# Kernel optimization log

Hardware: AMD Instinct MI355X
Metric: run time of the kernel (lower is better)

Reference implementation:

```python
import jax, jax.numpy as jnp
import numpy as np

H = 1024          # hidden_size
C = 4             # residual_channels
RH = 16           # residual_heads
HS = H // RH      # head_size for residual (64)
DR = 8            # delta_rank
M = 4096          # mlp_size
NH = 16           # attention heads
HD = H // NH      # attention head dim (64)
A_SIZE = (C - 1) * RH   # 48
B_SIZE = C * RH         # 64
EPS = 1e-5
SSM_EPS = 1e-5


def rat_read(res, W, gamma, beta, num_outputs):
    # res: [b,l,H*C]; W: [H, num_outputs, C] (Conv1d groups=H)
    b, l, _ = res.shape
    x = res.reshape(b, l, H, C)
    y = jnp.einsum('blhc,hoc->bloh', x, W)            # [b,l,o,H]
    mu = y.mean(-1, keepdims=True)
    var = y.var(-1, keepdims=True)
    yn = (y - mu) * jax.lax.rsqrt(var + EPS)          # GroupNorm: each group = one output
    yn = yn * gamma.reshape(num_outputs, H) + beta.reshape(num_outputs, H)
    return yn.reshape(b, l, num_outputs * H)


def rope(x, pos):
    # x: [b,l,NH,HD], pos: [b,l]
    half = HD // 2
    inv = 1.0 / (10000.0 ** (jnp.arange(half, dtype=jnp.float32) / half))
    ang = pos.astype(jnp.float32)[..., None] * inv    # [b,l,half]
    cos = jnp.cos(ang)[:, :, None, :]
    sin = jnp.sin(ang)[:, :, None, :]
    x1, x2 = x[..., :half], x[..., half:]
    return jnp.concatenate([x1 * cos - x2 * sin, x2 * cos + x1 * sin], axis=-1)


def attention(qkv_in, qkv_w, pos):
    # qkv_in: [b,l,3H]; qkv_w: [3,H,H] (grouped 1x1 conv = 3 independent linears)
    b, l, _ = qkv_in.shape
    q, k, v = jnp.split(qkv_in, 3, axis=-1)
    q = jnp.einsum('bli,oi->blo', q, qkv_w[0]).reshape(b, l, NH, HD)
    k = jnp.einsum('bli,oi->blo', k, qkv_w[1]).reshape(b, l, NH, HD)
    v = jnp.einsum('bli,oi->blo', v, qkv_w[2]).reshape(b, l, NH, HD)
    q = rope(q, pos)
    k = rope(k, pos)
    scores = jnp.einsum('bqhd,bkhd->bhqk', q, k) / np.sqrt(HD).astype(np.float32)
    mask = jnp.tril(jnp.ones((l, l), dtype=bool))
    scores = jnp.where(mask, scores, jnp.float32(-1e30))
    p = jax.nn.softmax(scores, axis=-1)
    o = jnp.einsum('bhqk,bkhd->bqhd', p, v)
    return o.reshape(b, l, H)  # get_o is identity (no output proj)


def rat_write(res, y, wod_w, wab_w, wab_b, du_w, du_b):
    # res: [b,l,H*C], y: [b,l,y_size]
    b, l, _ = res.shape
    o_d = y @ wod_w.T                                 # [b,l,H+DR]
    A_B = y @ wab_w.T + wab_b                         # [b,l,A+B]
    out = o_d[..., :H]
    delta_low = o_d[..., H:]
    A_logit = A_B[..., :A_SIZE]
    B_proj = A_B[..., A_SIZE:2 * A_SIZE]
    B_skip = A_B[..., 2 * A_SIZE:]
    delta = jax.nn.softplus(delta_low @ du_w.T + du_b)  # [b,l,H]
    hs = res.reshape(b, l, HS, RH, C)
    out = out.reshape(b, l, HS, RH, 1)
    delta = delta.reshape(b, l, HS, RH, 1)
    A_logit = A_logit.reshape(b, l, 1, RH, C - 1)
    B_proj = B_proj.reshape(b, l, 1, RH, C - 1)
    B_skip = B_skip.reshape(b, l, 1, RH, 1)
    A_neg = -jax.nn.softplus(A_logit)
    A_bar = jnp.exp(delta * A_neg)
    B_bar = (A_bar - 1.0) / (A_neg - SSM_EPS) * B_proj
    B_bar_skip = delta * B_skip
    A_full = jnp.concatenate([A_bar, jnp.ones_like(A_bar[..., :1])], axis=-1)
    B_full = jnp.concatenate([B_bar, B_bar_skip], axis=-1)
    return (hs * A_full + out * B_full).reshape(b, l, H * C)


def layer_forward(hidden_states, position_ids, attn_read_w, attn_read_g, attn_read_b,
                  qkv_w, attn_wod_w, attn_wab_w, attn_wab_b, attn_du_w, attn_du_b,
                  mlp_read_w, mlp_read_g, mlp_read_b, mlp_in_w,
                  mlp_wod_w, mlp_wab_w, mlp_wab_b, mlp_du_w, mlp_du_b):
    qkv_in = rat_read(hidden_states, attn_read_w, attn_read_g, attn_read_b, 3)
    attn_out = attention(qkv_in, qkv_w, position_ids)
    hidden_states = rat_write(hidden_states, attn_out, attn_wod_w, attn_wab_w,
                              attn_wab_b, attn_du_w, attn_du_b)
    mlp_in = rat_read(hidden_states, mlp_read_w, mlp_read_g, mlp_read_b, 2)
    g_in, u_in = mlp_in[..., :H], mlp_in[..., H:]
    gate = jnp.einsum('bli,oi->blo', g_in, mlp_in_w[0])
    up = jnp.einsum('bli,oi->blo', u_in, mlp_in_w[1])
    mlp_out = jax.nn.silu(gate) * up                  # [b,l,M]
    hidden_states = rat_write(hidden_states, mlp_out, mlp_wod_w, mlp_wab_w,
                              mlp_wab_b, mlp_du_w, mlp_du_b)
    return hidden_states


def setup_inputs() -> dict:
    key = jax.random.key(0)
    ks = jax.random.split(key, 20)
    B, L = 2, 2048
    s = 0.02
    return {
        'hidden_states': jax.random.normal(ks[0], (B, L, H * C), jnp.float32),
        'position_ids': jnp.tile(jnp.arange(L, dtype=jnp.int64), (B, 1)),
        'attn_read_w': jax.random.normal(ks[1], (H, 3, C), jnp.float32) / np.sqrt(C).astype(np.float32),
        'attn_read_g': jnp.ones((3 * H,), jnp.float32),
        'attn_read_b': jnp.zeros((3 * H,), jnp.float32),
        'qkv_w': jax.random.normal(ks[2], (3, H, H), jnp.float32) * s,
        'attn_wod_w': jax.random.normal(ks[3], (H + DR, H), jnp.float32) * s,
        'attn_wab_w': jax.random.normal(ks[4], (A_SIZE + B_SIZE, H), jnp.float32) * s,
        'attn_wab_b': jax.random.normal(ks[5], (A_SIZE + B_SIZE,), jnp.float32) * s,
        'attn_du_w': jax.random.normal(ks[6], (H, DR), jnp.float32) * s,
        'attn_du_b': jax.random.normal(ks[7], (H,), jnp.float32) * s,
        'mlp_read_w': jax.random.normal(ks[8], (H, 2, C), jnp.float32) / np.sqrt(C).astype(np.float32),
        'mlp_read_g': jnp.ones((2 * H,), jnp.float32),
        'mlp_read_b': jnp.zeros((2 * H,), jnp.float32),
        'mlp_in_w': jax.random.normal(ks[9], (2, M, H), jnp.float32) * s,
        'mlp_wod_w': jax.random.normal(ks[10], (H + DR, M), jnp.float32) * s,
        'mlp_wab_w': jax.random.normal(ks[11], (A_SIZE + B_SIZE, M), jnp.float32) * s,
        'mlp_wab_b': jax.random.normal(ks[12], (A_SIZE + B_SIZE,), jnp.float32) * s,
        'mlp_du_w': jax.random.normal(ks[13], (H, DR), jnp.float32) * s,
        'mlp_du_b': jax.random.normal(ks[14], (H,), jnp.float32) * s,
    }


def reference(hidden_states, position_ids, attn_read_w, attn_read_g, attn_read_b,
              qkv_w, attn_wod_w, attn_wab_w, attn_wab_b, attn_du_w, attn_du_b,
              mlp_read_w, mlp_read_g, mlp_read_b, mlp_in_w,
              mlp_wod_w, mlp_wab_w, mlp_wab_b, mlp_du_w, mlp_du_b):
    return layer_forward(hidden_states, position_ids, attn_read_w, attn_read_g,
                         attn_read_b, qkv_w, attn_wod_w, attn_wab_w, attn_wab_b,
                         attn_du_w, attn_du_b, mlp_read_w, mlp_read_g, mlp_read_b,
                         mlp_in_w, mlp_wod_w, mlp_wab_w, mlp_wab_b, mlp_du_w, mlp_du_b)
```

## Files before the change

### kernel.cpp

```cpp
#include <hip/hip_runtime.h>
#include <hip/hip_bf16.h>
#include <math.h>
#include <stdint.h>


constexpr int NTOK = 4096;

typedef __attribute__((ext_vector_type(8))) short short8_t;
typedef __attribute__((ext_vector_type(4))) float f32x4;

__device__ __forceinline__ ushort f2bf(float f) {
    union { float f; uint32_t u; } v; v.f = f;
    uint32_t r = v.u + 0x7fffu + ((v.u >> 16) & 1u);
    return (ushort)(r >> 16);
}
__device__ __forceinline__ float bf2f(ushort b) {
    union { uint32_t u; float f; } v; v.u = ((uint32_t)b) << 16;
    return v.f;
}
__device__ __forceinline__ uint32_t pack2(float lo, float hi) {
    union { __hip_bfloat162 h; uint32_t u; } v;
    v.h = __float22bfloat162_rn(make_float2(lo, hi));
    return v.u;
}
__device__ __forceinline__ float softplus_f(float x) {
    return (x > 20.0f) ? x : log1pf(expf(x));
}

__device__ __forceinline__ void gload_lds16(const void* g, void* l) {
    __builtin_amdgcn_global_load_lds(
        (const __attribute__((address_space(1))) uint32_t*)g,
        (__attribute__((address_space(3))) uint32_t*)l,
        16, 0, 0);
}

__global__ __launch_bounds__(256) void convert_flat_kernel(
    const float* __restrict__ src, ushort* __restrict__ dst)
{
    const size_t i = ((size_t)blockIdx.x * 256 + threadIdx.x) * 8;
    const float4 a = *(const float4*)(src + i);
    const float4 b = *(const float4*)(src + i + 4);
    union { ushort u[8]; uint4 v; } o;
    o.u[0] = f2bf(a.x); o.u[1] = f2bf(a.y); o.u[2] = f2bf(a.z); o.u[3] = f2bf(a.w);
    o.u[4] = f2bf(b.x); o.u[5] = f2bf(b.y); o.u[6] = f2bf(b.z); o.u[7] = f2bf(b.w);
    *(uint4*)(dst + i) = o.v;
}

__global__ __launch_bounds__(256) void rope_tab_kernel(float2* __restrict__ tab)
{
    const int idx = blockIdx.x * 256 + threadIdx.x;
    const int i = idx & 31;
    const int pos = idx >> 5;
    const float inv = expf(-(float)i * (9.210340371976184f / 32.0f));
    float s, c;
    sincosf((float)pos * inv, &s, &c);
    tab[idx] = make_float2(c, s);
}

__global__ __launch_bounds__(256) void build_comb_kernel(
    const float* __restrict__ wod, const float* __restrict__ wab,
    ushort* __restrict__ dst, int K)
{
    const size_t i = ((size_t)blockIdx.x * 256 + threadIdx.x) * 8;
    const int row = (int)(i / (size_t)K);
    const int col = (int)(i % (size_t)K);
    const float* src = nullptr;
    if (row < 1024)      src = wod + (size_t)row * K + col;
    else if (row < 1136) src = wab + (size_t)(row - 1024) * K + col;
    else if (row < 1144) src = wod + (size_t)(1024 + row - 1136) * K + col;
    union { ushort u[8]; uint4 v; } o;
    if (src) {
        const float4 a = *(const float4*)(src);
        const float4 b = *(const float4*)(src + 4);
        o.u[0] = f2bf(a.x); o.u[1] = f2bf(a.y); o.u[2] = f2bf(a.z); o.u[3] = f2bf(a.w);
        o.u[4] = f2bf(b.x); o.u[5] = f2bf(b.y); o.u[6] = f2bf(b.z); o.u[7] = f2bf(b.w);
    } else {
        o.v = make_uint4(0, 0, 0, 0);
    }
    *(uint4*)(dst + i) = o.v;
}

template <int NO>
__global__ __launch_bounds__(256) void rat_read_kernel(
    const float* __restrict__ res, const float* __restrict__ W,
    const float* __restrict__ gamma, const float* __restrict__ beta,
    ushort* __restrict__ out)
{
    const int t = blockIdx.x;
    const int tid = threadIdx.x;
    const float* rp = res + (size_t)t * 4096;
    float y[4][NO];
#pragma unroll
    for (int i = 0; i < 4; ++i) {
        const int h = tid + 256 * i;
        const float4 x = *(const float4*)(rp + h * 4);
#pragma unroll
        for (int o = 0; o < NO; ++o) {
            const float4 w = *(const float4*)(W + ((size_t)h * NO + o) * 4);
            y[i][o] = x.x * w.x + x.y * w.y + x.z * w.z + x.w * w.w;
        }
    }
    __shared__ float red[4][NO][2];
    const int lane = tid & 63, wid = tid >> 6;
#pragma unroll
    for (int o = 0; o < NO; ++o) {
        float s = 0.f, ss = 0.f;
#pragma unroll
        for (int i = 0; i < 4; ++i) { s += y[i][o]; ss += y[i][o] * y[i][o]; }
        for (int off = 32; off > 0; off >>= 1) {
            s += __shfl_down(s, off);
            ss += __shfl_down(ss, off);
        }
        if (lane == 0) { red[wid][o][0] = s; red[wid][o][1] = ss; }
    }
    __syncthreads();
    float mu[NO], rs[NO];
#pragma unroll
    for (int o = 0; o < NO; ++o) {
        const float s  = red[0][o][0] + red[1][o][0] + red[2][o][0] + red[3][o][0];
        const float ss = red[0][o][1] + red[1][o][1] + red[2][o][1] + red[3][o][1];
        const float m = s * (1.0f / 1024.0f);
        const float v = ss * (1.0f / 1024.0f) - m * m;
        mu[o] = m;
        rs[o] = rsqrtf(v + 1e-5f);
    }
    ushort* op = out + (size_t)t * (NO * 1024);
#pragma unroll
    for (int i = 0; i < 4; ++i) {
        const int h = tid + 256 * i;
#pragma unroll
        for (int o = 0; o < NO; ++o) {
            op[o * 1024 + h] = f2bf((y[i][o] - mu[o]) * rs[o] * gamma[o * 1024 + h] + beta[o * 1024 + h]);
        }
    }
}

__device__ __forceinline__ void stage_tile(
    ushort* AsB, ushort* BsB, const ushort* Ag, const ushort* Wg,
    size_t lda8, size_t ldw8, int w, int kofs)
{
#pragma unroll
    for (int i = 0; i < 4; ++i) {
        gload_lds16(Ag + kofs + i * lda8, AsB + (w * 4 + i) * 512);
        gload_lds16(Wg + kofs + i * ldw8, BsB + (w * 4 + i) * 512);
    }
}

template <int EPI>
__global__ __launch_bounds__(256) void mfma_gemm_kernel(
    const ushort* __restrict__ A, int lda,
    const ushort* __restrict__ W, int ldw,
    void* __restrict__ Cp, int ldc,
    const ushort* __restrict__ U,
    int Kblk)
{
    __shared__ ushort As[2][128 * 64];
    __shared__ ushort Bs[2][128 * 64];
    const int tid = threadIdx.x;
    const int nwg = gridDim.x * gridDim.y;
    const int gy = gridDim.y;
    const int id = blockIdx.y * gridDim.x + blockIdx.x;
    const int swz = (id & 7) * (nwg >> 3) + (id >> 3);
    const int bm = (swz / gy) * 128;
    const int bo = (swz % gy) * 128;

    const int w = tid >> 6, l = tid & 63;
    const int lq = l & 15, lg = l >> 4;
    const int wr = (w >> 1) * 64, wc = (w & 1) * 64;

    f32x4 acc[4][4];
#pragma unroll
    for (int i = 0; i < 4; ++i)
#pragma unroll
        for (int j = 0; j < 4; ++j) acc[i][j] = (f32x4){0.f, 0.f, 0.f, 0.f};

    const int srow = 32 * w + (l >> 3);
    const int skc  = ((l & 7) ^ (l >> 3)) * 8;
    const ushort* Ag = A + (size_t)(bm + srow) * lda + (size_t)blockIdx.z * Kblk + skc;
    const ushort* Wg = W + (size_t)(bo + srow) * ldw + (size_t)blockIdx.z * Kblk + skc;
    const size_t lda8 = (size_t)8 * lda, ldw8 = (size_t)8 * ldw;

    const int nt = Kblk >> 6;
    stage_tile(As[0], Bs[0], Ag, Wg, lda8, ldw8, w, 0);
    __syncthreads();
    int cur = 0;
    for (int t = 0; t < nt; ++t) {
        if (t + 1 < nt)
            stage_tile(As[cur ^ 1], Bs[cur ^ 1], Ag, Wg, lda8, ldw8, w, (t + 1) * 64);
#pragma unroll
        for (int ks = 0; ks < 2; ++ks) {
            short8_t af[4], bf[4];
            const int jc = ks * 4 + lg;
#pragma unroll
            for (int mf = 0; mf < 4; ++mf) {
                const int ra = wr + mf * 16 + lq;
                af[mf] = *(const short8_t*)&As[cur][ra * 64 + ((jc ^ (ra & 7)) * 8)];
                const int rb = wc + mf * 16 + lq;
                bf[mf] = *(const short8_t*)&Bs[cur][rb * 64 + ((jc ^ (rb & 7)) * 8)];
            }
#pragma unroll
            for (int mf = 0; mf < 4; ++mf)
#pragma unroll
                for (int nf = 0; nf < 4; ++nf)
                    acc[mf][nf] = __builtin_amdgcn_mfma_f32_16x16x32_bf16(
                        af[mf], bf[nf], acc[mf][nf], 0, 0, 0);
        }
        __syncthreads();
        cur ^= 1;
    }

    ushort* eb = &As[0][0] + w * 4096;
#pragma unroll
    for (int mf = 0; mf < 4; ++mf)
#pragma unroll
        for (int r = 0; r < 4; ++r)
#pragma unroll
            for (int nf = 0; nf < 4; ++nf) {
                const int rl = mf * 16 + lg * 4 + r;
                const int cl = nf * 16 + lq;
                eb[rl * 64 + cl] = f2bf(acc[mf][nf][r]);
            }
#pragma unroll
    for (int p = 0; p < 8; ++p) {
        const int rl = p * 8 + (l >> 3);
        const int cl = (l & 7) * 8;
        const uint4 v = *(const uint4*)&eb[rl * 64 + cl];
        ushort* dst = (ushort*)Cp + ((size_t)blockIdx.z * NTOK + bm + wr + rl) * ldc + bo + wc + cl;
        *(uint4*)dst = v;
    }
}

template <int EPI>
__global__ __launch_bounds__(512) void gemm256_kernel(
    const ushort* __restrict__ A, int lda,
    const ushort* __restrict__ W, int ldw,
    ushort* __restrict__ Cp, int ldc,
    const ushort* __restrict__ U, int K)
{
    __shared__ ushort lds[2][2][256 * 32];
    const int tid = threadIdx.x;
    const int nwg = gridDim.x * gridDim.y;
    const int gy = gridDim.y;
    const int id = blockIdx.y * gridDim.x + blockIdx.x;
    const int swz = (id & 7) * (nwg >> 3) + (id >> 3);
    const int bm = (swz / gy) * 256;
    const int bo = (swz % gy) * 256;

    const int w = tid >> 6, l = tid & 63;
    const int lq = l & 15, lg = l >> 4;
    const int wrow = (w >> 2) * 128, wcol = (w & 3) * 64;

    f32x4 acc[8][4];
#pragma unroll
    for (int i = 0; i < 8; ++i)
#pragma unroll
        for (int j = 0; j < 4; ++j) acc[i][j] = (f32x4){0.f, 0.f, 0.f, 0.f};

    const int srow = w * 32 + (l >> 2);
    const int schunk = (l & 3) ^ ((l >> 3) & 3);
    const ushort* Ag = A + (size_t)(bm + srow) * lda + schunk * 8;
    const ushort* Wg = W + (size_t)(bo + srow) * ldw + schunk * 8;
    const size_t lda16 = (size_t)16 * lda, ldw16 = (size_t)16 * ldw;

    const int nt = K >> 5;
    int cur = 0;
#pragma unroll
    for (int i = 0; i < 2; ++i) {
        gload_lds16(Ag + i * lda16, &lds[0][0][(w * 32 + i * 16) * 32]);
        gload_lds16(Wg + i * ldw16, &lds[0][1][(w * 32 + i * 16) * 32]);
    }
    __syncthreads();
    for (int t = 0; t < nt; ++t) {
        if (t + 1 < nt) {
            const int k0 = (t + 1) * 32;
#pragma unroll
            for (int i = 0; i < 2; ++i) {
                gload_lds16(Ag + k0 + i * lda16, &lds[cur ^ 1][0][(w * 32 + i * 16) * 32]);
                gload_lds16(Wg + k0 + i * ldw16, &lds[cur ^ 1][1][(w * 32 + i * 16) * 32]);
            }
        }
        short8_t af[8], bf[4];
#pragma unroll
        for (int mf = 0; mf < 8; ++mf) {
            const int ra = wrow + mf * 16 + lq;
            af[mf] = *(const short8_t*)&lds[cur][0][ra * 32 + ((lg ^ ((ra >> 1) & 3)) * 8)];
        }
#pragma unroll
        for (int nf = 0; nf < 4; ++nf) {
            const int rb = wcol + nf * 16 + lq;
            bf[nf] = *(const short8_t*)&lds[cur][1][rb * 32 + ((lg ^ ((rb >> 1) & 3)) * 8)];
        }
        __builtin_amdgcn_s_setprio(1);
#pragma unroll
        for (int mf = 0; mf < 8; ++mf)
#pragma unroll
            for (int nf = 0; nf < 4; ++nf)
                acc[mf][nf] = __builtin_amdgcn_mfma_f32_16x16x32_bf16(
                    af[mf], bf[nf], acc[mf][nf], 0, 0, 0);
        __builtin_amdgcn_s_setprio(0);
        __syncthreads();
        cur ^= 1;
    }

    ushort* eb = &lds[0][0][0] + w * 4096;
#pragma unroll
    for (int h = 0; h < 2; ++h) {
#pragma unroll
        for (int mf2 = 0; mf2 < 4; ++mf2)
#pragma unroll
            for (int r = 0; r < 4; ++r)
#pragma unroll
                for (int nf = 0; nf < 4; ++nf) {
                    const int rl = mf2 * 16 + lg * 4 + r;
                    const int cl = nf * 16 + lq;
                    eb[rl * 64 + cl] = f2bf(acc[h * 4 + mf2][nf][r]);
                }
#pragma unroll
        for (int p = 0; p < 8; ++p) {
            const int rl = p * 8 + (l >> 3);
            const int cl = (l & 7) * 8;
            const uint4 v = *(const uint4*)&eb[rl * 64 + cl];
            const size_t row = bm + wrow + h * 64 + rl;
            const size_t col = bo + wcol + cl;
            if (EPI == 1) {
                *(uint4*)(Cp + row * ldc + col) = v;
            } else {
                const uint4 uv = *(const uint4*)(U + row * ldc + col);
                union { uint4 v; ushort u[8]; } g, uu, o;
                g.v = v; uu.v = uv;
#pragma unroll
                for (int e = 0; e < 8; ++e) {
                    const float gf = bf2f(g.u[e]);
                    o.u[e] = f2bf(gf / (1.0f + __expf(-gf)) * bf2f(uu.u[e]));
                }
                *(uint4*)(Cp + row * ldc + col) = o.v;
            }
        }
    }
}

__global__ __launch_bounds__(256) void qkv_gemm_kernel(
    const ushort* __restrict__ Ain, const ushort* __restrict__ Wall,
    const float2* __restrict__ rtab,
    ushort* __restrict__ Qb, ushort* __restrict__ Kb, ushort* __restrict__ Vt)
{
    __shared__ ushort As[2][128 * 64];
    __shared__ ushort Bs[2][128 * 64];
    const int tid = threadIdx.x;
    const int z = blockIdx.z;
    const int nwg = gridDim.x * gridDim.y;
    const int gy = gridDim.y;
    const int id = blockIdx.y * gridDim.x + blockIdx.x;
    const int swz = (id & 7) * (nwg >> 3) + (id >> 3);
    const int bm = (swz / gy) * 128;
    const int bo = (swz % gy) * 128;

    const int w = tid >> 6, l = tid & 63;
    const int lq = l & 15, lg = l >> 4;
    const int wr = (w >> 1) * 64, wc = (w & 1) * 64;

    f32x4 acc[4][4];
#pragma unroll
    for (int i = 0; i < 4; ++i)
#pragma unroll
        for (int j = 0; j < 4; ++j) acc[i][j] = (f32x4){0.f, 0.f, 0.f, 0.f};

    const int srow = 32 * w + (l >> 3);
    const int skc  = ((l & 7) ^ (l >> 3)) * 8;
    const ushort* Ag = Ain + z * 1024 + (size_t)(bm + srow) * 3072 + skc;
    const ushort* Wg = Wall + (size_t)z * 1048576 + (size_t)(bo + srow) * 1024 + skc;
    const size_t lda8 = (size_t)8 * 3072, ldw8 = (size_t)8 * 1024;

    stage_tile(As[0], Bs[0], Ag, Wg, lda8, ldw8, w, 0);
    __syncthreads();
    int cur = 0;
    for (int t = 0; t < 16; ++t) {
        if (t + 1 < 16)
            stage_tile(As[cur ^ 1], Bs[cur ^ 1], Ag, Wg, lda8, ldw8, w, (t + 1) * 64);
#pragma unroll
        for (int ks = 0; ks < 2; ++ks) {
            short8_t af[4], bf[4];
            const int jc = ks * 4 + lg;
#pragma unroll
            for (int mf = 0; mf < 4; ++mf) {
                const int ra = wr + mf * 16 + lq;
                af[mf] = *(const short8_t*)&As[cur][ra * 64 + ((jc ^ (ra & 7)) * 8)];
                const int rb = wc + mf * 16 + lq;
                bf[mf] = *(const short8_t*)&Bs[cur][rb * 64 + ((jc ^ (rb & 7)) * 8)];
            }
#pragma unroll
            for (int mf = 0; mf < 4; ++mf)
#pragma unroll
                for (int nf = 0; nf < 4; ++nf)
                    acc[mf][nf] = __builtin_amdgcn_mfma_f32_16x16x32_bf16(
                        af[mf], bf[nf], acc[mf][nf], 0, 0, 0);
        }
        __syncthreads();
        cur ^= 1;
    }

    if (z < 2) {
        ushort* Out = z ? Kb : Qb;
        const float scale = z ? 1.0f : 0.18033688f;
        const int cbase = bo + wc;
#pragma unroll
        for (int mf = 0; mf < 4; ++mf)
#pragma unroll
            for (int r = 0; r < 4; ++r) {
                const int row = bm + wr + mf * 16 + lg * 4 + r;
                const int pos = row & 2047;
#pragma unroll
                for (int nf = 0; nf < 2; ++nf) {
                    const int i = nf * 16 + lq;
                    const float2 cs = rtab[pos * 32 + i];
                    const float x1 = acc[mf][nf][r];
                    const float x2 = acc[mf][nf + 2][r];
                    Out[(size_t)row * 1024 + cbase + i]      = f2bf((x1 * cs.x - x2 * cs.y) * scale);
                    Out[(size_t)row * 1024 + cbase + i + 32] = f2bf((x2 * cs.x + x1 * cs.y) * scale);
                }
            }
    } else {
        ushort* eb = &As[0][0] + w * 4096;
#pragma unroll
        for (int mf = 0; mf < 4; ++mf)
#pragma unroll
            for (int r = 0; r < 4; ++r)
#pragma unroll
                for (int nf = 0; nf < 4; ++nf) {
                    const int rl = mf * 16 + lg * 4 + r;
                    const int cl = nf * 16 + lq;
                    eb[cl * 64 + rl] = f2bf(acc[mf][nf][r]);
                }
#pragma unroll
        for (int p = 0; p < 8; ++p) {
            const int rl = p * 8 + (l >> 3);
            const int cl = (l & 7) * 8;
            const uint4 v = *(const uint4*)&eb[rl * 64 + cl];
            *(uint4*)(Vt + (size_t)(bo + wc + rl) * NTOK + bm + wr + cl) = v;
        }
    }
}

__global__ __launch_bounds__(256) void attn_mfma_kernel(
    const ushort* __restrict__ Qb, const ushort* __restrict__ Kb,
    const ushort* __restrict__ Vt, ushort* __restrict__ atno)
{
    __shared__ ushort Ks[2][2][64 * 64];
    __shared__ ushort Vs[2][2][64 * 64];
    const int bh = blockIdx.y;
    const int b = bh >> 4, h = bh & 15;
    const int w = threadIdx.x >> 6, l = threadIdx.x & 63;
    const int g = l >> 4, t = l & 15;
    const int tok0 = b * 2048;
    const int hoff = h * 64;

    const int srow = w * 16 + (l >> 3);
    const int schunk = (l & 7) ^ (l >> 3);
    const ushort* Kg = Kb + (size_t)(tok0 + srow) * 1024 + hoff + schunk * 8;
    const ushort* Vg = Vt + (size_t)(hoff + srow) * NTOK + tok0 + schunk * 8;
    const int ldsbase = w * 1024;

    const int srcA = ((g & 1) * 2) * 16 + t;
    const int srcB = srcA + 16;
    const bool hiSel = (g >> 1) != 0;

    const int q0 = 31 - blockIdx.x;
    const int q1 = blockIdx.x;
    const int nt0 = (q0 + 2) >> 1;
    const int nt1 = (q1 + 2) >> 1;
    const int qabs[2] = {q0 * 64 + w * 16 + t, q1 * 64 + w * 16 + t};

    short8_t qf[2][2];
#pragma unroll
    for (int ks = 0; ks < 2; ++ks) {
        qf[0][ks] = *(const short8_t*)(Qb + (size_t)(tok0 + q0 * 64 + w * 16 + t) * 1024 + hoff + ks * 32 + g * 8);
        qf[1][ks] = *(const short8_t*)(Qb + (size_t)(tok0 + q1 * 64 + w * 16 + t) * 1024 + hoff + ks * 32 + g * 8);
    }

    float m_run[2] = {-3.0e38f, -3.0e38f};
    float l_run[2] = {0.0f, 0.0f};
    f32x4 oacc[2][4];
#pragma unroll
    for (int qi = 0; qi < 2; ++qi)
#pragma unroll
        for (int nf = 0; nf < 4; ++nf) oacc[qi][nf] = (f32x4){0.f, 0.f, 0.f, 0.f};

#pragma unroll
    for (int hf = 0; hf < 2; ++hf)
#pragma unroll
        for (int i = 0; i < 2; ++i) {
            gload_lds16(Kg + (size_t)(hf * 64 + i * 8) * 1024, &Ks[0][hf][ldsbase + i * 512]);
            gload_lds16(Vg + hf * 64 + (size_t)(i * 8) * NTOK, &Vs[0][hf][ldsbase + i * 512]);
        }
    __syncthreads();

    int buf = 0;
    for (int kt = 0; kt < nt0; ++kt) {
        if (kt + 1 < nt0) {
            const int nk = (kt + 1) * 128;
#pragma unroll
            for (int hf = 0; hf < 2; ++hf)
#pragma unroll
                for (int i = 0; i < 2; ++i) {
                    gload_lds16(Kg + (size_t)(nk + hf * 64 + i * 8) * 1024, &Ks[buf ^ 1][hf][ldsbase + i * 512]);
                    gload_lds16(Vg + nk + hf * 64 + (size_t)(i * 8) * NTOK, &Vs[buf ^ 1][hf][ldsbase + i * 512]);
                }
        }
#pragma unroll
        for (int qi = 0; qi < 2; ++qi) {
            if (qi == 1 && kt >= nt1) break;
            const int ntq = qi ? nt1 : nt0;
            f32x4 sa[2][4];
#pragma unroll
            for (int hf = 0; hf < 2; ++hf)
#pragma unroll
                for (int mf = 0; mf < 4; ++mf) sa[hf][mf] = (f32x4){0.f, 0.f, 0.f, 0.f};
            __builtin_amdgcn_s_setprio(1);
#pragma unroll
            for (int hf = 0; hf < 2; ++hf)
#pragma unroll
                for (int ks = 0; ks < 2; ++ks) {
                    const int jc = ks * 4 + g;
#pragma unroll
                    for (int mf = 0; mf < 4; ++mf) {
                        const short8_t kf = *(const short8_t*)&Ks[buf][hf][(mf * 16 + t) * 64 + ((jc ^ (t & 7)) * 8)];
                        sa[hf][mf] = __builtin_amdgcn_mfma_f32_16x16x32_bf16(kf, qf[qi][ks], sa[hf][mf], 0, 0, 0);
                    }
                }
            __builtin_amdgcn_s_setprio(0);

            float p[2][4][4];
            float mloc = -3.0e38f;
            const bool lastTile = (kt == ntq - 1);
#pragma unroll
            for (int hf = 0; hf < 2; ++hf)
#pragma unroll
                for (int mf = 0; mf < 4; ++mf)
#pragma unroll
                    for (int r = 0; r < 4; ++r) {
                        float s = sa[hf][mf][r];
                        if (lastTile && (kt * 128 + hf * 64 + mf * 16 + g * 4 + r) > qabs[qi]) s = -3.0e38f;
                        p[hf][mf][r] = s;
                        mloc = fmaxf(mloc, s);
                    }
            mloc = fmaxf(mloc, __shfl_xor(mloc, 16));
            mloc = fmaxf(mloc, __shfl_xor(mloc, 32));
            const float mnew = fmaxf(m_run[qi], mloc);
            float lsum = 0.f;
#pragma unroll
            for (int hf = 0; hf < 2; ++hf)
#pragma unroll
                for (int mf = 0; mf < 4; ++mf)
#pragma unroll
                    for (int r = 0; r < 4; ++r) {
                        const float e = exp2f(p[hf][mf][r] - mnew);
                        p[hf][mf][r] = e;
                        lsum += e;
                    }
            lsum += __shfl_xor(lsum, 16);
            lsum += __shfl_xor(lsum, 32);
            const float fac = exp2f(m_run[qi] - mnew);
            l_run[qi] = l_run[qi] * fac + lsum;
            m_run[qi] = mnew;
#pragma unroll
            for (int r = 0; r < 4; ++r) {
                const float fr = __shfl(fac, g * 4 + r);
#pragma unroll
                for (int nf = 0; nf < 4; ++nf) oacc[qi][nf][r] *= fr;
            }
#pragma unroll
            for (int hf = 0; hf < 2; ++hf) {
                uint32_t pk[4][2];
#pragma unroll
                for (int mf = 0; mf < 4; ++mf) {
                    pk[mf][0] = pack2(p[hf][mf][0], p[hf][mf][1]);
                    pk[mf][1] = pack2(p[hf][mf][2], p[hf][mf][3]);
                }
#pragma unroll
                for (int ks = 0; ks < 2; ++ks) {
                    const uint32_t a00 = __shfl(pk[2 * ks][0], srcA);
                    const uint32_t a01 = __shfl(pk[2 * ks][1], srcA);
                    const uint32_t a10 = __shfl(pk[2 * ks + 1][0], srcA);
                    const uint32_t a11 = __shfl(pk[2 * ks + 1][1], srcA);
                    const uint32_t b00 = __shfl(pk[2 * ks][0], srcB);
                    const uint32_t b01 = __shfl(pk[2 * ks][1], srcB);
                    const uint32_t b10 = __shfl(pk[2 * ks + 1][0], srcB);
                    const uint32_t b11 = __shfl(pk[2 * ks + 1][1], srcB);
                    union { uint32_t u[4]; short8_t v; } pa;
                    pa.u[0] = hiSel ? a10 : a00;
                    pa.u[1] = hiSel ? a11 : a01;
                    pa.u[2] = hiSel ? b10 : b00;
                    pa.u[3] = hiSel ? b11 : b01;
                    const int jc = ks * 4 + g;
                    __builtin_amdgcn_s_setprio(1);
#pragma unroll
                    for (int nf = 0; nf < 4; ++nf) {
                        const short8_t vf = *(const short8_t*)&Vs[buf][hf][(nf * 16 + t) * 64 + ((jc ^ (t & 7)) * 8)];
                        oacc[qi][nf] = __builtin_amdgcn_mfma_f32_16x16x32_bf16(pa.v, vf, oacc[qi][nf], 0, 0, 0);
                    }
                    __builtin_amdgcn_s_setprio(0);
                }
            }
        }
        __syncthreads();
        buf ^= 1;
    }

#pragma unroll
    for (int qi = 0; qi < 2; ++qi) {
        const float inv = 1.0f / l_run[qi];
        const int qb = qi ? q1 : q0;
#pragma unroll
        for (int r = 0; r < 4; ++r) {
            const float ir = __shfl(inv, g * 4 + r);
            const int orow = tok0 + qb * 64 + w * 16 + g * 4 + r;
#pragma unroll
            for (int nf = 0; nf < 4; ++nf)
                atno[(size_t)orow * 1024 + hoff + nf * 16 + t] = f2bf(oacc[qi][nf][r] * ir);
        }
    }
}

template <int FUSE_READ>
__global__ __launch_bounds__(256) void rat_write_kernel(
    const float* __restrict__ res, const ushort* __restrict__ part,
    const float* __restrict__ wab_b, const float* __restrict__ du_w,
    const float* __restrict__ du_b, float* __restrict__ out,
    const float* __restrict__ Wr, const float* __restrict__ gamma,
    const float* __restrict__ beta, ushort* __restrict__ mlp_in)
{
    const int t = blockIdx.x;
    const int tid = threadIdx.x;
    const size_t zs = (size_t)NTOK * 1152;
    const ushort* p0 = part + (size_t)t * 1152;
    __shared__ float sAB[112];
    __shared__ float sdl[8];
    __shared__ float sA2[48];
    __shared__ float sBf[48];
    __shared__ float sBs[16];
    if (tid < 112)
        sAB[tid] = bf2f(p0[1024 + tid]) + bf2f(p0[zs + 1024 + tid])
                 + bf2f(p0[2 * zs + 1024 + tid]) + bf2f(p0[3 * zs + 1024 + tid]) + wab_b[tid];
    if (tid >= 128 && tid < 136) {
        const int j = tid - 128;
        sdl[j] = bf2f(p0[1136 + j]) + bf2f(p0[zs + 1136 + j])
               + bf2f(p0[2 * zs + 1136 + j]) + bf2f(p0[3 * zs + 1136 + j]);
    }
    __syncthreads();
    if (tid < 48) {
        const float Aneg = -softplus_f(sAB[tid]);
        sA2[tid] = Aneg * 1.4426950408889634f;
        sBf[tid] = sAB[48 + tid] / (Aneg - 1e-5f);
    } else if (tid >= 64 && tid < 80) {
        sBs[tid - 64] = sAB[96 + (tid - 64)];
    }
    __syncthreads();
    const float* rp = res + (size_t)t * 4096;
    float* op = out + (size_t)t * 4096;
    float y[4][2];
#pragma unroll
    for (int ii = 0; ii < 4; ++ii) {
        const int hh = tid + 256 * ii;
        const int rh = hh & 15;
        const float4 w0 = *(const float4*)(du_w + hh * 8);
        const float4 w1 = *(const float4*)(du_w + hh * 8 + 4);
        float dacc = du_b[hh];
        dacc += sdl[0] * w0.x + sdl[1] * w0.y + sdl[2] * w0.z + sdl[3] * w0.w;
        dacc += sdl[4] * w1.x + sdl[5] * w1.y + sdl[6] * w1.z + sdl[7] * w1.w;
        const float delta = softplus_f(dacc);
        const float oh = bf2f(p0[hh]) + bf2f(p0[zs + hh]) + bf2f(p0[2 * zs + hh]) + bf2f(p0[3 * zs + hh]);
        const float4 hs = *(const float4*)(rp + hh * 4);
        const float r4[4] = {hs.x, hs.y, hs.z, hs.w};
        float o4[4];
#pragma unroll
        for (int c = 0; c < 3; ++c) {
            const float Abar = exp2f(delta * sA2[rh * 3 + c]);
            o4[c] = r4[c] * Abar + oh * (Abar - 1.0f) * sBf[rh * 3 + c];
        }
        o4[3] = r4[3] + oh * (delta * sBs[rh]);
        *(float4*)(op + hh * 4) = make_float4(o4[0], o4[1], o4[2], o4[3]);
        if (FUSE_READ) {
#pragma unroll
            for (int o = 0; o < 2; ++o) {
                const float4 w = *(const float4*)(Wr + ((size_t)hh * 2 + o) * 4);
                y[ii][o] = o4[0] * w.x + o4[1] * w.y + o4[2] * w.z + o4[3] * w.w;
            }
        }
    }
    if (FUSE_READ) {
        __shared__ float red[4][2][2];
        const int lane = tid & 63, wid = tid >> 6;
#pragma unroll
        for (int o = 0; o < 2; ++o) {
            float s = 0.f, ss = 0.f;
#pragma unroll
            for (int i = 0; i < 4; ++i) { s += y[i][o]; ss += y[i][o] * y[i][o]; }
            for (int off = 32; off > 0; off >>= 1) {
                s += __shfl_down(s, off);
                ss += __shfl_down(ss, off);
            }
            if (lane == 0) { red[wid][o][0] = s; red[wid][o][1] = ss; }
        }
        __syncthreads();
        float mu[2], rs[2];
#pragma unroll
        for (int o = 0; o < 2; ++o) {
            const float s  = red[0][o][0] + red[1][o][0] + red[2][o][0] + red[3][o][0];
            const float ss = red[0][o][1] + red[1][o][1] + red[2][o][1] + red[3][o][1];
            const float m = s * (1.0f / 1024.0f);
            const float v = ss * (1.0f / 1024.0f) - m * m;
            mu[o] = m;
            rs[o] = rsqrtf(v + 1e-5f);
        }
        ushort* mp = mlp_in + (size_t)t * 2048;
#pragma unroll
        for (int i = 0; i < 4; ++i) {
            const int h = tid + 256 * i;
#pragma unroll
            for (int o = 0; o < 2; ++o)
                mp[o * 1024 + h] = f2bf((y[i][o] - mu[o]) * rs[o] * gamma[o * 1024 + h] + beta[o * 1024 + h]);
        }
    }
}

extern "C" void kernel_launch(void* const* d_in, const int* in_sizes, int n_in,
                              void* d_out, int out_size, void* d_ws, size_t ws_size,
                              hipStream_t stream)
{
    const float* hidden      = (const float*)d_in[0];
    const float* attn_read_w = (const float*)d_in[2];
    const float* attn_read_g = (const float*)d_in[3];
    const float* attn_read_b = (const float*)d_in[4];
    const float* qkv_w       = (const float*)d_in[5];
    const float* attn_wod_w  = (const float*)d_in[6];
    const float* attn_wab_w  = (const float*)d_in[7];
    const float* attn_wab_b  = (const float*)d_in[8];
    const float* attn_du_w   = (const float*)d_in[9];
    const float* attn_du_b   = (const float*)d_in[10];
    const float* mlp_read_w  = (const float*)d_in[11];
    const float* mlp_read_g  = (const float*)d_in[12];
    const float* mlp_read_b  = (const float*)d_in[13];
    const float* mlp_in_w    = (const float*)d_in[14];
    const float* mlp_wod_w   = (const float*)d_in[15];
    const float* mlp_wab_w   = (const float*)d_in[16];
    const float* mlp_wab_b   = (const float*)d_in[17];
    const float* mlp_du_w    = (const float*)d_in[18];
    const float* mlp_du_b    = (const float*)d_in[19];
    float* out = (float*)d_out;
    char* wsb = (char*)d_ws;
    const size_t N = NTOK;

    ushort* qkv_wb  = (ushort*)(wsb + 0);
    ushort* wcombA  = (ushort*)(wsb + 6291456);
    ushort* mlpin_b = (ushort*)(wsb + 8650752);
    ushort* wcombM  = (ushort*)(wsb + 25427968);
    float2* rtab    = (float2*)(wsb + 34865152);
    char* R1 = wsb + 35389440;
    char* R2 = wsb + 60555264;
    ushort* qkv_in = (ushort*)R1;
    ushort* mlp_in = (ushort*)R1;
    ushort* Qb   = (ushort*)R2;
    ushort* Kb   = (ushort*)(R2 + 8388608);
    ushort* atno = (ushort*)(R2 + 16777216);
    ushort* Vt   = (ushort*)(R2 + 33554432);
    ushort* pA   = (ushort*)(R2 + 25165824);
    ushort* upb  = (ushort*)R2;
    ushort* up_  = (ushort*)(R2 + 33554432);
    ushort* pM   = (ushort*)(R2 + 33554432);

    convert_flat_kernel<<<1536, 256, 0, stream>>>(qkv_w, qkv_wb);
    convert_flat_kernel<<<4096, 256, 0, stream>>>(mlp_in_w, mlpin_b);
    build_comb_kernel<<<576, 256, 0, stream>>>(attn_wod_w, attn_wab_w, wcombA, 1024);
    build_comb_kernel<<<2304, 256, 0, stream>>>(mlp_wod_w, mlp_wab_w, wcombM, 4096);
    rope_tab_kernel<<<256, 256, 0, stream>>>(rtab);

    rat_read_kernel<3><<<N, 256, 0, stream>>>(hidden, attn_read_w, attn_read_g, attn_read_b, qkv_in);

    qkv_gemm_kernel<<<dim3(32, 8, 3), 256, 0, stream>>>(qkv_in, qkv_wb, rtab, Qb, Kb, Vt);

    attn_mfma_kernel<<<dim3(16, 32), 256, 0, stream>>>(Qb, Kb, Vt, atno);

    mfma_gemm_kernel<4><<<dim3(32, 9, 4), 256, 0, stream>>>(atno, 1024, wcombA, 1024, pA, 1152, nullptr, 256);

    rat_write_kernel<1><<<N, 256, 0, stream>>>(hidden, pA, attn_wab_b, attn_du_w, attn_du_b, out,
                                               mlp_read_w, mlp_read_g, mlp_read_b, mlp_in);

    gemm256_kernel<1><<<dim3(16, 16), 512, 0, stream>>>(mlp_in + 1024, 2048, mlpin_b + 4194304, 1024, up_, 4096, nullptr, 1024);
    gemm256_kernel<2><<<dim3(16, 16), 512, 0, stream>>>(mlp_in, 2048, mlpin_b, 1024, upb, 4096, up_, 1024);

    mfma_gemm_kernel<4><<<dim3(32, 9, 4), 256, 0, stream>>>(upb, 4096, wcombM, 4096, pM, 1152, nullptr, 1024);

    rat_write_kernel<0><<<N, 256, 0, stream>>>(out, pM, mlp_wab_b, mlp_du_w, mlp_du_b, out,
                                               nullptr, nullptr, nullptr, nullptr);
}
```

Measured before the change: 408.5 us.

## Split attention query tiles across 8 waves instead of looping per wave

```diff
diff --git a/kernel.cpp b/kernel.cpp
--- a/kernel.cpp
+++ b/kernel.cpp
@@ -441,7 +441,7 @@
     }
 }
 
-__global__ __launch_bounds__(256) void attn_mfma_kernel(
+__global__ __launch_bounds__(512) void attn_mfma_kernel(
     const ushort* __restrict__ Qb, const ushort* __restrict__ Kb,
     const ushort* __restrict__ Vt, ushort* __restrict__ atno)
 {
@@ -449,16 +449,17 @@
     __shared__ ushort Vs[2][2][64 * 64];
     const int bh = blockIdx.y;
     const int b = bh >> 4, h = bh & 15;
-    const int w = threadIdx.x >> 6, l = threadIdx.x & 63;
+    const int tid = threadIdx.x;
+    const int w = tid >> 6, l = tid & 63;
     const int g = l >> 4, t = l & 15;
     const int tok0 = b * 2048;
     const int hoff = h * 64;
 
-    const int srow = w * 16 + (l >> 3);
+    const int srow = w * 8 + (l >> 3);
     const int schunk = (l & 7) ^ (l >> 3);
     const ushort* Kg = Kb + (size_t)(tok0 + srow) * 1024 + hoff + schunk * 8;
     const ushort* Vg = Vt + (size_t)(hoff + srow) * NTOK + tok0 + schunk * 8;
-    const int ldsbase = w * 1024;
+    const int ldsbase = w * 512;
 
     const int srcA = ((g & 1) * 2) * 16 + t;
     const int srcB = srcA + 16;
@@ -467,31 +468,27 @@
     const int q0 = 31 - blockIdx.x;
     const int q1 = blockIdx.x;
     const int nt0 = (q0 + 2) >> 1;
-    const int nt1 = (q1 + 2) >> 1;
-    const int qabs[2] = {q0 * 64 + w * 16 + t, q1 * 64 + w * 16 + t};
-
-    short8_t qf[2][2];
-#pragma unroll
-    for (int ks = 0; ks < 2; ++ks) {
-        qf[0][ks] = *(const short8_t*)(Qb + (size_t)(tok0 + q0 * 64 + w * 16 + t) * 1024 + hoff + ks * 32 + g * 8);
-        qf[1][ks] = *(const short8_t*)(Qb + (size_t)(tok0 + q1 * 64 + w * 16 + t) * 1024 + hoff + ks * 32 + g * 8);
-    }
-
-    float m_run[2] = {-3.0e38f, -3.0e38f};
-    float l_run[2] = {0.0f, 0.0f};
-    f32x4 oacc[2][4];
-#pragma unroll
-    for (int qi = 0; qi < 2; ++qi)
-#pragma unroll
-        for (int nf = 0; nf < 4; ++nf) oacc[qi][nf] = (f32x4){0.f, 0.f, 0.f, 0.f};
-
-#pragma unroll
-    for (int hf = 0; hf < 2; ++hf)
-#pragma unroll
-        for (int i = 0; i < 2; ++i) {
-            gload_lds16(Kg + (size_t)(hf * 64 + i * 8) * 1024, &Ks[0][hf][ldsbase + i * 512]);
-            gload_lds16(Vg + hf * 64 + (size_t)(i * 8) * NTOK, &Vs[0][hf][ldsbase + i * 512]);
-        }
+    const int qi = w >> 2;
+    const int wq = w & 3;
+    const int qb = qi ? q1 : q0;
+    const int ntq = (qb + 2) >> 1;
+    const int qabs = qb * 64 + wq * 16 + t;
+
+    short8_t qf[2];
+#pragma unroll
+    for (int ks = 0; ks < 2; ++ks)
+        qf[ks] = *(const short8_t*)(Qb + (size_t)(tok0 + qabs) * 1024 + hoff + ks * 32 + g * 8);
+
+    float m_run = -3.0e38f, l_run = 0.0f;
+    f32x4 oacc[4];
+#pragma unroll
+    for (int nf = 0; nf < 4; ++nf) oacc[nf] = (f32x4){0.f, 0.f, 0.f, 0.f};
+
+#pragma unroll
+    for (int hf = 0; hf < 2; ++hf) {
+        gload_lds16(Kg + (size_t)(hf * 64) * 1024, &Ks[0][hf][ldsbase]);
+        gload_lds16(Vg + hf * 64, &Vs[0][hf][ldsbase]);
+    }
     __syncthreads();
 
     int buf = 0;
@@ -499,17 +496,12 @@
         if (kt + 1 < nt0) {
             const int nk = (kt + 1) * 128;
 #pragma unroll
-            for (int hf = 0; hf < 2; ++hf)
-#pragma unroll
-                for (int i = 0; i < 2; ++i) {
-                    gload_lds16(Kg + (size_t)(nk + hf * 64 + i * 8) * 1024, &Ks[buf ^ 1][hf][ldsbase + i * 512]);
-                    gload_lds16(Vg + nk + hf * 64 + (size_t)(i * 8) * NTOK, &Vs[buf ^ 1][hf][ldsbase + i * 512]);
-                }
-        }
-#pragma unroll
-        for (int qi = 0; qi < 2; ++qi) {
-            if (qi == 1 && kt >= nt1) break;
-            const int ntq = qi ? nt1 : nt0;
+            for (int hf = 0; hf < 2; ++hf) {
+                gload_lds16(Kg + (size_t)(nk + hf * 64) * 1024, &Ks[buf ^ 1][hf][ldsbase]);
+                gload_lds16(Vg + nk + hf * 64, &Vs[buf ^ 1][hf][ldsbase]);
+            }
+        }
+        if (kt < ntq) {
             f32x4 sa[2][4];
 #pragma unroll
             for (int hf = 0; hf < 2; ++hf)
@@ -524,7 +516,7 @@
 #pragma unroll
                     for (int mf = 0; mf < 4; ++mf) {
                         const short8_t kf = *(const short8_t*)&Ks[buf][hf][(mf * 16 + t) * 64 + ((jc ^ (t & 7)) * 8)];
-                        sa[hf][mf] = __builtin_amdgcn_mfma_f32_16x16x32_bf16(kf, qf[qi][ks], sa[hf][mf], 0, 0, 0);
+                        sa[hf][mf] = __builtin_amdgcn_mfma_f32_16x16x32_bf16(kf, qf[ks], sa[hf][mf], 0, 0, 0);
                     }
                 }
             __builtin_amdgcn_s_setprio(0);
@@ -539,13 +531,13 @@
 #pragma unroll
                     for (int r = 0; r < 4; ++r) {
                         float s = sa[hf][mf][r];
-                        if (lastTile && (kt * 128 + hf * 64 + mf * 16 + g * 4 + r) > qabs[qi]) s = -3.0e38f;
+                        if (lastTile && (kt * 128 + hf * 64 + mf * 16 + g * 4 + r) > qabs) s = -3.0e38f;
                         p[hf][mf][r] = s;
                         mloc = fmaxf(mloc, s);
                     }
             mloc = fmaxf(mloc, __shfl_xor(mloc, 16));
             mloc = fmaxf(mloc, __shfl_xor(mloc, 32));
-            const float mnew = fmaxf(m_run[qi], mloc);
+            const float mnew = fmaxf(m_run, mloc);
             float lsum = 0.f;
 #pragma unroll
             for (int hf = 0; hf < 2; ++hf)
@@ -559,14 +551,14 @@
                     }
             lsum += __shfl_xor(lsum, 16);
             lsum += __shfl_xor(lsum, 32);
-            const float fac = exp2f(m_run[qi] - mnew);
-            l_run[qi] = l_run[qi] * fac + lsum;
-            m_run[qi] = mnew;
+            const float fac = exp2f(m_run - mnew);
+            l_run = l_run * fac + lsum;
+            m_run = mnew;
 #pragma unroll
             for (int r = 0; r < 4; ++r) {
                 const float fr = __shfl(fac, g * 4 + r);
 #pragma unroll
-                for (int nf = 0; nf < 4; ++nf) oacc[qi][nf][r] *= fr;
+                for (int nf = 0; nf < 4; ++nf) oacc[nf][r] *= fr;
             }
 #pragma unroll
             for (int hf = 0; hf < 2; ++hf) {
@@ -596,7 +588,7 @@
 #pragma unroll
                     for (int nf = 0; nf < 4; ++nf) {
                         const short8_t vf = *(const short8_t*)&Vs[buf][hf][(nf * 16 + t) * 64 + ((jc ^ (t & 7)) * 8)];
-                        oacc[qi][nf] = __builtin_amdgcn_mfma_f32_16x16x32_bf16(pa.v, vf, oacc[qi][nf], 0, 0, 0);
+                        oacc[nf] = __builtin_amdgcn_mfma_f32_16x16x32_bf16(pa.v, vf, oacc[nf], 0, 0, 0);
                     }
                     __builtin_amdgcn_s_setprio(0);
                 }
@@ -606,18 +598,14 @@
         buf ^= 1;
     }
 
-#pragma unroll
-    for (int qi = 0; qi < 2; ++qi) {
-        const float inv = 1.0f / l_run[qi];
-        const int qb = qi ? q1 : q0;
-#pragma unroll
-        for (int r = 0; r < 4; ++r) {
-            const float ir = __shfl(inv, g * 4 + r);
-            const int orow = tok0 + qb * 64 + w * 16 + g * 4 + r;
-#pragma unroll
-            for (int nf = 0; nf < 4; ++nf)
-                atno[(size_t)orow * 1024 + hoff + nf * 16 + t] = f2bf(oacc[qi][nf][r] * ir);
-        }
+    const float inv = 1.0f / l_run;
+#pragma unroll
+    for (int r = 0; r < 4; ++r) {
+        const float ir = __shfl(inv, g * 4 + r);
+        const int orow = tok0 + qb * 64 + wq * 16 + g * 4 + r;
+#pragma unroll
+        for (int nf = 0; nf < 4; ++nf)
+            atno[(size_t)orow * 1024 + hoff + nf * 16 + t] = f2bf(oacc[nf][r] * ir);
     }
 }
 
@@ -778,7 +766,7 @@
 
     qkv_gemm_kernel<<<dim3(32, 8, 3), 256, 0, stream>>>(qkv_in, qkv_wb, rtab, Qb, Kb, Vt);
 
-    attn_mfma_kernel<<<dim3(16, 32), 256, 0, stream>>>(Qb, Kb, Vt, atno);
+    attn_mfma_kernel<<<dim3(16, 32), 512, 0, stream>>>(Qb, Kb, Vt, atno);
 
     mfma_gemm_kernel<4><<<dim3(32, 9, 4), 256, 0, stream>>>(atno, 1024, wcombA, 1024, pA, 1152, nullptr, 256);
 
```

Measured after the change: 406.1 us. No clear change (-0.6%).
